# Performance work log

Measured on AMD Instinct MI355X. Metric: run time of the kernel, lower is better.

## Reference

```python
import jax, jax.numpy as jnp
import numpy as np

MIN_R, MAX_R = -51.2, 51.2
ORIG_W, ORIG_H = 800.0, 448.0


def sample_bilinear(feat, gx, gy):
    # feat [N,C,H,W]; gx,gy [N,Q] in grid coords [-1,1], align_corners=True, zeros padding
    N, C, H, W = feat.shape
    px = (gx + 1.0) * 0.5 * (W - 1)
    py = (gy + 1.0) * 0.5 * (H - 1)
    x0 = jnp.floor(px)
    y0 = jnp.floor(py)
    x0i = x0.astype(jnp.int32)
    y0i = y0.astype(jnp.int32)
    wx1 = px - x0
    wy1 = py - y0
    ff = feat.reshape(N, C, H * W)

    def corner(xi, yi, w):
        valid = (xi >= 0) & (xi < W) & (yi >= 0) & (yi < H)
        idx = jnp.clip(yi, 0, H - 1) * W + jnp.clip(xi, 0, W - 1)
        vals = jax.vmap(lambda f, i: f[:, i])(ff, idx)  # [N,C,Q]
        return vals * (w * valid.astype(w.dtype))[:, None, :]

    return (corner(x0i, y0i, (1 - wx1) * (1 - wy1))
            + corner(x0i + 1, y0i, wx1 * (1 - wy1))
            + corner(x0i, y0i + 1, (1 - wx1) * wy1)
            + corner(x0i + 1, y0i + 1, wx1 * wy1))


def setup_inputs() -> dict:
    key = jax.random.key(0)
    ks = jax.random.split(key, 16)
    B, Q, C, N = 2, 900, 256, 6
    levels = [(112, 200), (56, 100), (28, 50), (14, 25)]
    inp = {
        'query': jax.random.normal(ks[0], (B, Q, C), jnp.float32),
        'reference_points': jax.random.uniform(ks[1], (B, Q, 3), jnp.float32),
        'key_padding_mask': jax.random.bernoulli(ks[2], 0.1, (B, Q)),
        'cam_intrinsics': jax.random.normal(ks[3], (B, N, 3, 3), jnp.float32),
        'cam_extrinsics': jax.random.normal(ks[4], (B, N, 4, 4), jnp.float32),
    }
    for li, (h, w) in enumerate(levels):
        inp[f'feats_l{li}'] = jax.random.normal(ks[5 + li], (B, N, C, h, w), jnp.float32)
    inp['Wq'] = jax.random.normal(ks[10], (C, C), jnp.float32) * 0.02
    inp['bq'] = jnp.zeros((C,), jnp.float32)
    inp['Wv'] = jax.random.normal(ks[11], (C, C), jnp.float32) * 0.02
    inp['bv'] = jnp.zeros((C,), jnp.float32)
    inp['Wo'] = jax.random.normal(ks[12], (C, C), jnp.float32) * 0.02
    inp['bo'] = jnp.zeros((C,), jnp.float32)
    return inp


def reference(query, reference_points, key_padding_mask, cam_intrinsics, cam_extrinsics,
              feats_l0, feats_l1, feats_l2, feats_l3, Wq, bq, Wv, bv, Wo, bo):
    B, Q, C = query.shape
    N = cam_extrinsics.shape[1]
    mask = key_padding_mask

    ref = reference_points * (MAX_R - MIN_R) + MIN_R
    ref = jnp.where(mask[..., None], jnp.float32(-1000.0), ref)

    q = query @ Wq.T + bq

    ref_hom = jnp.concatenate([ref, jnp.ones((B, Q, 1), ref.dtype)], axis=-1)  # [B,Q,4]
    inv_ext = jnp.nan_to_num(jnp.linalg.inv(cam_extrinsics), nan=0.0, posinf=1e6, neginf=-1e6)
    # per-cam: points_cam_hom = ref_hom @ inv_ext^T  -> [B,N,Q,4]
    pts_cam_hom = jnp.einsum('bqj,bnij->bnqi', ref_hom, inv_ext)
    depth = jnp.nan_to_num(pts_cam_hom[..., 2:3], nan=10.0, posinf=100.0, neginf=-100.0)
    invalid = depth[..., 0] < 1.5  # [B,N,Q]
    depth_safe = jnp.maximum(depth, 1.5)
    pts_cam = pts_cam_hom[..., :3] / depth_safe
    pts_img = jnp.einsum('bnqj,bnij->bnqi', pts_cam, cam_intrinsics)[..., :2]
    pts_img = jnp.clip(pts_img, -3000.0, 3000.0)  # [B,N,Q,2]

    level_sum = jnp.zeros((B * N, C, Q), jnp.float32)
    for feat in (feats_l0, feats_l1, feats_l2, feats_l3):
        Hf, Wf = feat.shape[3], feat.shape[4]
        fx = pts_img[..., 0] * (Wf / ORIG_W)
        fy = pts_img[..., 1] * (Hf / ORIG_H)
        gx = jnp.clip(fx / (Wf - 1.0) * 2.0 - 1.0, -10.0, 10.0)
        gy = jnp.clip(fy / (Hf - 1.0) * 2.0 - 1.0, -10.0, 10.0)
        gx = jnp.where(invalid, jnp.float32(-100.0), gx)
        gy = jnp.where(invalid, jnp.float32(-100.0), gy)
        s = sample_bilinear(feat.reshape(B * N, C, Hf, Wf),
                            gx.reshape(B * N, Q), gy.reshape(B * N, Q))
        level_sum = level_sum + jnp.nan_to_num(s)

    ms = (level_sum / 4.0).reshape(B, N, C, Q).transpose(0, 1, 3, 2)  # [B,N,Q,C]
    v = ms @ Wv.T + bv
    sampled = jnp.max(v, axis=1)  # max over cameras -> [B,Q,C]

    fused = jax.nn.relu(q + sampled) + q
    out = fused @ Wo.T + bo
    out = out * (~mask)[..., None].astype(out.dtype)
    return out
```

## Files before the change

kernel.cpp:

```cpp
#include <hip/hip_runtime.h>
#include <hip/hip_bf16.h>
#include <math.h>

#define BB 2
#define NCAM 6
#define NQ 900
#define NC 256
#define BN (BB*NCAM)
#define NROW (BB*NQ)

typedef float f4 __attribute__((ext_vector_type(4)));
typedef unsigned short u16x4 __attribute__((ext_vector_type(4)));

__device__ __forceinline__ float u2f(unsigned short u){
  union{unsigned int v; float fl;} x; x.v=((unsigned int)u)<<16; return x.fl;
}

template<int F>
__device__ __forceinline__ float ld1(const void* p, long i){
  if (F) return u2f(((const unsigned short*)p)[i]);
  return ((const float*)p)[i];
}
template<int F>
__device__ __forceinline__ f4 ld4(const void* p, long i){
  if (F){
    u16x4 u = *(const u16x4*)((const unsigned short*)p + i);
    f4 r; r.x=u2f(u.x); r.y=u2f(u.y); r.z=u2f(u.z); r.w=u2f(u.w); return r;
  }
  return *(const f4*)((const float*)p + i);
}

__global__ void prep_kernel(const unsigned char* __restrict__ refraw,
                            const void* __restrict__ ext,
                            const unsigned char* __restrict__ mask_raw,
                            int* __restrict__ flag_out,
                            float* __restrict__ inv_out,
                            int* __restrict__ mask_out){
  __shared__ int s_nonalign, s_gt1, s_bf, s_flag;
  int t = threadIdx.x;
  if (t==0){
    s_nonalign=0; s_gt1=0; s_bf=0;
    int cnt=0;
    for (int i=1;i<64;i+=4){
      unsigned char b = refraw[i];
      if (b>=0x30 && b<0x40) cnt++;
    }
    s_flag = (cnt>=12) ? 1 : 0;
    *flag_out = s_flag;
  }
  __syncthreads();
  int f_na=0, f_gt=0, f_bf=0;
  for (int i=t;i<NROW;i+=blockDim.x){
    unsigned char b = mask_raw[i];
    if ((i&3)!=0 && b!=0) f_na=1;
    if (b>1) f_gt=1;
    if ((i&3)==1 && b==0x3f) f_bf=1;
  }
  if (f_na) atomicOr(&s_nonalign,1);
  if (f_gt) atomicOr(&s_gt1,1);
  if (f_bf) atomicOr(&s_bf,1);
  __syncthreads();
  int fmt;
  if (!s_nonalign) fmt=0;
  else if (!s_gt1)  fmt=1;
  else              fmt = s_bf ? 2 : 3;
  for (int i=t;i<NROW;i+=blockDim.x){
    int v;
    if (fmt==0)      v = (((const int*)mask_raw)[i]            != 0);
    else if (fmt==1) v = (mask_raw[i]                          != 0);
    else if (fmt==2) v = (((const unsigned short*)mask_raw)[i] != 0);
    else             v = (((const float*)mask_raw)[i]          != 0.0f);
    mask_out[i]=v;
  }
  if (t < BN){
    int f = s_flag;
    double a[4][8];
    for(int i=0;i<4;i++){
      for(int j=0;j<4;j++) a[i][j] = (double)(f? u2f(((const unsigned short*)ext)[t*16+i*4+j])
                                               : ((const float*)ext)[t*16+i*4+j]);
      for(int j=0;j<4;j++) a[i][4+j] = (i==j)?1.0:0.0;
    }
    for(int col=0;col<4;col++){
      int piv=col; double best=fabs(a[col][col]);
      for(int r=col+1;r<4;r++){ double v=fabs(a[r][col]); if(v>best){best=v;piv=r;} }
      if(piv!=col) for(int j=0;j<8;j++){ double tmp=a[col][j]; a[col][j]=a[piv][j]; a[piv][j]=tmp; }
      double id = 1.0/a[col][col];
      for(int j=0;j<8;j++) a[col][j]*=id;
      for(int r=0;r<4;r++) if(r!=col){
        double fc=a[r][col];
        for(int j=0;j<8;j++) a[r][j]-=fc*a[col][j];
      }
    }
    for(int i=0;i<4;i++)for(int j=0;j<4;j++){
      float v=(float)a[i][4+j];
      if (isnan(v)) v=0.f;
      else if (isinf(v)) v = (v>0.f)?1e6f:-1e6f;
      inv_out[t*16+i*4+j]=v;
    }
  }
}

__global__ __launch_bounds__(256) void relayout_kernel(
    const void* __restrict__ Wq, const void* __restrict__ Wv,
    const void* __restrict__ Wo, const int* __restrict__ flag,
    float* __restrict__ dst){
  int e = blockIdx.x*256 + threadIdx.x;
  int f = *flag;
  int mat = e >> 16;
  int i = e & 65535;
  int t = i >> 8, k = i & 255;
  const void* W = (mat==0)?Wq:((mat==1)?Wv:Wo);
  float v = f ? u2f(((const unsigned short*)W)[i]) : ((const float*)W)[i];
  dst[mat*65536 + (k>>2)*1024 + t*4 + (k&3)] = v;
}

struct SharedMem {
  float q[NC];
  float ms[NCAM][NC];
  float fus[NC];
  float px[NCAM], py[NCAM];
  int   iv[NCAM];
  int   off[NCAM*4][4];
  float wgt[NCAM*4][4];
};

template<int F, int RL>
__device__ __forceinline__ void fused_body(
    const void* __restrict__ query, const void* __restrict__ refpts,
    const void* __restrict__ intr,
    const void* __restrict__ f0, const void* __restrict__ f1,
    const void* __restrict__ f2, const void* __restrict__ f3,
    const void* __restrict__ Wq, const void* __restrict__ bq,
    const void* __restrict__ Wv, const void* __restrict__ bv,
    const void* __restrict__ Wo, const void* __restrict__ bo,
    const float* __restrict__ Wblk,
    const float* __restrict__ inv_ext, const int* __restrict__ mask_int,
    float* __restrict__ out, SharedMem& sm){
  int row = blockIdx.x;
  int b = row/NQ;
  int t = threadIdx.x;
  int m = mask_int[row];

  const f4* Wq4 = (const f4*)(Wblk);
  const f4* Wv4 = (const f4*)(Wblk + 65536);
  const f4* Wo4 = (const f4*)(Wblk + 131072);

  sm.q[t] = ld1<F>(query, (long)row*NC+t);
  if (t < NCAM){
    float h0 = ld1<F>(refpts,(long)row*3+0)*102.4f - 51.2f;
    float h1 = ld1<F>(refpts,(long)row*3+1)*102.4f - 51.2f;
    float h2 = ld1<F>(refpts,(long)row*3+2)*102.4f - 51.2f;
    if (m){ h0=-1000.f; h1=-1000.f; h2=-1000.f; }
    const float* M = inv_ext + (b*NCAM+t)*16;
    float c0 = M[0]*h0 + M[1]*h1 + M[2]*h2 + M[3];
    float c1 = M[4]*h0 + M[5]*h1 + M[6]*h2 + M[7];
    float c2 = M[8]*h0 + M[9]*h1 + M[10]*h2 + M[11];
    float depth = c2;
    if (isnan(depth)) depth = 10.f;
    else if (isinf(depth)) depth = (depth>0)?100.f:-100.f;
    int iv = (depth < 1.5f);
    float ds = fmaxf(depth, 1.5f);
    float pc0=c0/ds, pc1=c1/ds, pc2=c2/ds;
    long kb = (long)(b*NCAM+t)*9;
    float ix = ld1<F>(intr,kb+0)*pc0 + ld1<F>(intr,kb+1)*pc1 + ld1<F>(intr,kb+2)*pc2;
    float iy = ld1<F>(intr,kb+3)*pc0 + ld1<F>(intr,kb+4)*pc1 + ld1<F>(intr,kb+5)*pc2;
    sm.px[t] = fminf(fmaxf(ix,-3000.f),3000.f);
    sm.py[t] = fminf(fmaxf(iy,-3000.f),3000.f);
    sm.iv[t] = iv;
  }
  __syncthreads();

  if (t < NCAM*4){
    const int Ws_[4]={200,100,50,25}, Hs_[4]={112,56,28,14};
    int n=t>>2, l=t&3;
    float x=sm.px[n], y=sm.py[n];
    int iv=sm.iv[n];
    int W=Ws_[l], H=Hs_[l];
    float gx = (x * ((float)W/800.f)) / (W-1.f) * 2.f - 1.f;
    float gy = (y * ((float)H/448.f)) / (H-1.f) * 2.f - 1.f;
    gx=fminf(fmaxf(gx,-10.f),10.f); gy=fminf(fmaxf(gy,-10.f),10.f);
    if(iv){gx=-100.f;gy=-100.f;}
    float pxx=(gx+1.f)*0.5f*(W-1.f);
    float pyy=(gy+1.f)*0.5f*(H-1.f);
    float x0f=floorf(pxx), y0f=floorf(pyy);
    int x0=(int)x0f, y0=(int)y0f;
    float wx1=pxx-x0f, wy1=pyy-y0f, wx0=1.f-wx1, wy0=1.f-wy1;
    int vx0=(x0>=0)&(x0<W), vx1=(x0+1>=0)&(x0+1<W);
    int vy0=(y0>=0)&(y0<H), vy1=(y0+1>=0)&(y0+1<H);
    int cx0=min(max(x0,0),W-1), cx1=min(max(x0+1,0),W-1);
    int cy0=min(max(y0,0),H-1), cy1=min(max(y0+1,0),H-1);
    sm.off[t][0]=cy0*W+cx0; sm.wgt[t][0]=wx0*wy0*(float)(vx0&vy0);
    sm.off[t][1]=cy0*W+cx1; sm.wgt[t][1]=wx1*wy0*(float)(vx1&vy0);
    sm.off[t][2]=cy1*W+cx0; sm.wgt[t][2]=wx0*wy1*(float)(vx0&vy1);
    sm.off[t][3]=cy1*W+cx1; sm.wgt[t][3]=wx1*wy1*(float)(vx1&vy1);
  }
  __syncthreads();

  {
    const void* fb[4]={f0,f1,f2,f3};
    const long HWs[4]={22400,5600,1400,350};
    #pragma unroll
    for(int n=0;n<NCAM;n++){
      int chan = (b*NCAM+n)*NC + t;
      float acc=0.f;
      #pragma unroll
      for(int l=0;l<4;l++){
        int u=n*4+l;
        long cb=(long)chan*HWs[l];
        const void* fp=fb[l];
        acc=fmaf(sm.wgt[u][0], ld1<F>(fp,cb+sm.off[u][0]), acc);
        acc=fmaf(sm.wgt[u][1], ld1<F>(fp,cb+sm.off[u][1]), acc);
        acc=fmaf(sm.wgt[u][2], ld1<F>(fp,cb+sm.off[u][2]), acc);
        acc=fmaf(sm.wgt[u][3], ld1<F>(fp,cb+sm.off[u][3]), acc);
      }
      sm.ms[n][t]=acc*0.25f;
    }
  }

  float qv = 0.f;
  {
    const f4* sq4=(const f4*)sm.q;
    #pragma unroll 8
    for(int k4=0;k4<NC/4;k4++){
      f4 wv = RL ? Wq4[k4*256 + t] : ld4<F>(Wq, (long)t*NC + 4*k4);
      f4 xv = sq4[k4];
      qv=fmaf(wv.x,xv.x,qv); qv=fmaf(wv.y,xv.y,qv);
      qv=fmaf(wv.z,xv.z,qv); qv=fmaf(wv.w,xv.w,qv);
    }
    qv += ld1<F>(bq,t);
  }
  __syncthreads();

  float ac[NCAM];
  #pragma unroll
  for(int n=0;n<NCAM;n++) ac[n]=0.f;
  {
    #pragma unroll 4
    for(int k4=0;k4<NC/4;k4++){
      f4 wv = RL ? Wv4[k4*256 + t] : ld4<F>(Wv, (long)t*NC + 4*k4);
      #pragma unroll
      for(int n=0;n<NCAM;n++){
        f4 mv=((const f4*)sm.ms[n])[k4];
        ac[n]=fmaf(wv.x,mv.x,ac[n]); ac[n]=fmaf(wv.y,mv.y,ac[n]);
        ac[n]=fmaf(wv.z,mv.z,ac[n]); ac[n]=fmaf(wv.w,mv.w,ac[n]);
      }
    }
  }
  float sv = ac[0];
  #pragma unroll
  for(int n=1;n<NCAM;n++) sv = fmaxf(sv, ac[n]);
  sv += ld1<F>(bv,t);

  sm.fus[t] = fmaxf(qv+sv, 0.f) + qv;
  __syncthreads();

  float o = 0.f;
  {
    const f4* sf4=(const f4*)sm.fus;
    #pragma unroll 8
    for(int k4=0;k4<NC/4;k4++){
      f4 wv = RL ? Wo4[k4*256 + t] : ld4<F>(Wo, (long)t*NC + 4*k4);
      f4 xv = sf4[k4];
      o=fmaf(wv.x,xv.x,o); o=fmaf(wv.y,xv.y,o);
      o=fmaf(wv.z,xv.z,o); o=fmaf(wv.w,xv.w,o);
    }
    o += ld1<F>(bo,t);
  }
  if (m) o = 0.f;
  out[(long)row*NC+t] = o;
}

template<int RL>
__global__ __launch_bounds__(256,4) void fused_kernel(
    const void* query, const void* refpts, const void* intr,
    const void* f0, const void* f1, const void* f2, const void* f3,
    const void* Wq, const void* bq, const void* Wv, const void* bv,
    const void* Wo, const void* bo, const float* __restrict__ Wblk,
    const float* __restrict__ inv_ext, const int* __restrict__ mask_int,
    const int* __restrict__ flag, float* __restrict__ out){
  __shared__ SharedMem sm;
  if (*flag)
    fused_body<1,RL>(query,refpts,intr,f0,f1,f2,f3,Wq,bq,Wv,bv,Wo,bo,Wblk,inv_ext,mask_int,out,sm);
  else
    fused_body<0,RL>(query,refpts,intr,f0,f1,f2,f3,Wq,bq,Wv,bv,Wo,bo,Wblk,inv_ext,mask_int,out,sm);
}

extern "C" void kernel_launch(void* const* d_in, const int* in_sizes, int n_in,
                              void* d_out, int out_size, void* d_ws, size_t ws_size,
                              hipStream_t stream){
  const void* query  = d_in[0];
  const void* refpts = d_in[1];
  const unsigned char* mask_raw = (const unsigned char*)d_in[2];
  const void* intr   = d_in[3];
  const void* ext    = d_in[4];
  const void* f0     = d_in[5];
  const void* f1     = d_in[6];
  const void* f2     = d_in[7];
  const void* f3     = d_in[8];
  const void* Wq     = d_in[9];
  const void* bq     = d_in[10];
  const void* Wv     = d_in[11];
  const void* bv     = d_in[12];
  const void* Wo     = d_in[13];
  const void* bo     = d_in[14];

  char* ws = (char*)d_ws;
  float* inv_ext  = (float*)(ws + 0);
  int*   dflag    = (int*)  (ws + 1024);
  int*   mask_int = (int*)  (ws + 2048);
  float* Wblk     = (float*)(ws + 16384);

  hipLaunchKernelGGL(prep_kernel, dim3(1), dim3(256), 0, stream,
                     (const unsigned char*)refpts, ext, mask_raw, dflag, inv_ext, mask_int);

  bool relay = ws_size >= (size_t)(16384 + 786432);
  if (relay){
    hipLaunchKernelGGL(relayout_kernel, dim3(768), dim3(256), 0, stream,
                       Wq, Wv, Wo, dflag, Wblk);
    hipLaunchKernelGGL(fused_kernel<1>, dim3(NROW), dim3(256), 0, stream,
                       query, refpts, intr, f0, f1, f2, f3,
                       Wq, bq, Wv, bv, Wo, bo, Wblk,
                       inv_ext, mask_int, dflag, (float*)d_out);
  } else {
    hipLaunchKernelGGL(fused_kernel<0>, dim3(NROW), dim3(256), 0, stream,
                       query, refpts, intr, f0, f1, f2, f3,
                       Wq, bq, Wv, bv, Wo, bo, Wblk,
                       inv_ext, mask_int, dflag, (float*)d_out);
  }
}
```

Before: 542.5 us.

## Process two rows per block, transpose small feature levels channel-last, merge prep kernels

Each block now handles two query rows, so every weight vector loaded for the Wq, Wv and Wo matvecs is reused across both rows. All 16 bilinear gather loads per camera are issued up front, before any accumulation. Feature levels 2 and 3 are transposed into a channel-contiguous workspace buffer in the prep kernel, so the sampling gathers become coalesced across threads. The prep, weight relayout and feature transposes are merged into one launch. The cost is extra per-call transpose traffic (about 17 MB written), higher shared-memory and register use per block, and half as many blocks.

```diff
diff --git a/kernel.cpp b/kernel.cpp
--- a/kernel.cpp
+++ b/kernel.cpp
@@ -8,6 +8,12 @@
 #define NC 256
 #define BN (BB*NCAM)
 #define NROW (BB*NQ)
+#define RPB 2
+
+#define HW0 22400
+#define HW1 5600
+#define HW2 1400
+#define HW3 350
 
 typedef float f4 __attribute__((ext_vector_type(4)));
 typedef unsigned short u16x4 __attribute__((ext_vector_type(4)));
@@ -30,25 +36,63 @@
   return *(const f4*)((const float*)p + i);
 }
 
-__global__ void prep_kernel(const unsigned char* __restrict__ refraw,
-                            const void* __restrict__ ext,
-                            const unsigned char* __restrict__ mask_raw,
-                            int* __restrict__ flag_out,
-                            float* __restrict__ inv_out,
-                            int* __restrict__ mask_out){
-  __shared__ int s_nonalign, s_gt1, s_bf, s_flag;
+__device__ __forceinline__ int sniff_flag(const unsigned char* refraw){
+  int cnt=0;
+  for (int i=1;i<64;i+=4){
+    unsigned char b = refraw[i];
+    if (b>=0x30 && b<0x40) cnt++;
+  }
+  return (cnt>=12) ? 1 : 0;
+}
+
+__global__ __launch_bounds__(256) void prep_all(
+    const unsigned char* __restrict__ refraw,
+    const void* __restrict__ ext,
+    const unsigned char* __restrict__ mask_raw,
+    const void* __restrict__ Wq, const void* __restrict__ Wv,
+    const void* __restrict__ Wo,
+    const void* __restrict__ f2, const void* __restrict__ f3,
+    int nW, int nT2, int nT3,
+    int* __restrict__ flag_out, float* __restrict__ inv_out,
+    int* __restrict__ mask_out,
+    float* __restrict__ Wblk, float* __restrict__ T2buf,
+    float* __restrict__ T3buf){
+  __shared__ int sflag, s_na, s_gt, s_bf;
   int t = threadIdx.x;
-  if (t==0){
-    s_nonalign=0; s_gt1=0; s_bf=0;
-    int cnt=0;
-    for (int i=1;i<64;i+=4){
-      unsigned char b = refraw[i];
-      if (b>=0x30 && b<0x40) cnt++;
-    }
-    s_flag = (cnt>=12) ? 1 : 0;
-    *flag_out = s_flag;
-  }
-  __syncthreads();
+  int bi = blockIdx.x;
+  if (t==0){ sflag = sniff_flag(refraw); s_na=0; s_gt=0; s_bf=0; }
+  __syncthreads();
+  int f = sflag;
+
+  if (bi < nW){
+    int e = bi*256 + t;
+    int mat = e >> 16;
+    int i = e & 65535;
+    int tt = i >> 8, k = i & 255;
+    const void* W = (mat==0)?Wq:((mat==1)?Wv:Wo);
+    float v = f ? u2f(((const unsigned short*)W)[i]) : ((const float*)W)[i];
+    Wblk[mat*65536 + (k>>2)*1024 + tt*4 + (k&3)] = v;
+    return;
+  }
+  if (bi < nW+nT2){
+    int e = (bi-nW)*256 + t;
+    int bn = e / (HW2*NC);
+    int rem = e - bn*(HW2*NC);
+    int p = rem >> 8, c = rem & 255;
+    int src = (bn*NC + c)*HW2 + p;
+    T2buf[e] = f ? u2f(((const unsigned short*)f2)[src]) : ((const float*)f2)[src];
+    return;
+  }
+  if (bi < nW+nT2+nT3){
+    int e = (bi-nW-nT2)*256 + t;
+    int bn = e / (HW3*NC);
+    int rem = e - bn*(HW3*NC);
+    int p = rem >> 8, c = rem & 255;
+    int src = (bn*NC + c)*HW3 + p;
+    T3buf[e] = f ? u2f(((const unsigned short*)f3)[src]) : ((const float*)f3)[src];
+    return;
+  }
+
   int f_na=0, f_gt=0, f_bf=0;
   for (int i=t;i<NROW;i+=blockDim.x){
     unsigned char b = mask_raw[i];
@@ -56,14 +100,14 @@
     if (b>1) f_gt=1;
     if ((i&3)==1 && b==0x3f) f_bf=1;
   }
-  if (f_na) atomicOr(&s_nonalign,1);
-  if (f_gt) atomicOr(&s_gt1,1);
+  if (f_na) atomicOr(&s_na,1);
+  if (f_gt) atomicOr(&s_gt,1);
   if (f_bf) atomicOr(&s_bf,1);
   __syncthreads();
   int fmt;
-  if (!s_nonalign) fmt=0;
-  else if (!s_gt1)  fmt=1;
-  else              fmt = s_bf ? 2 : 3;
+  if (!s_na) fmt=0;
+  else if (!s_gt) fmt=1;
+  else fmt = s_bf ? 2 : 3;
   for (int i=t;i<NROW;i+=blockDim.x){
     int v;
     if (fmt==0)      v = (((const int*)mask_raw)[i]            != 0);
@@ -72,8 +116,8 @@
     else             v = (((const float*)mask_raw)[i]          != 0.0f);
     mask_out[i]=v;
   }
+  if (t==0) *flag_out = f;
   if (t < BN){
-    int f = s_flag;
     double a[4][8];
     for(int i=0;i<4;i++){
       for(int j=0;j<4;j++) a[i][j] = (double)(f? u2f(((const unsigned short*)ext)[t*16+i*4+j])
@@ -100,31 +144,17 @@
   }
 }
 
-__global__ __launch_bounds__(256) void relayout_kernel(
-    const void* __restrict__ Wq, const void* __restrict__ Wv,
-    const void* __restrict__ Wo, const int* __restrict__ flag,
-    float* __restrict__ dst){
-  int e = blockIdx.x*256 + threadIdx.x;
-  int f = *flag;
-  int mat = e >> 16;
-  int i = e & 65535;
-  int t = i >> 8, k = i & 255;
-  const void* W = (mat==0)?Wq:((mat==1)?Wv:Wo);
-  float v = f ? u2f(((const unsigned short*)W)[i]) : ((const float*)W)[i];
-  dst[mat*65536 + (k>>2)*1024 + t*4 + (k&3)] = v;
-}
-
 struct SharedMem {
-  float q[NC];
-  float ms[NCAM][NC];
-  float fus[NC];
-  float px[NCAM], py[NCAM];
-  int   iv[NCAM];
-  int   off[NCAM*4][4];
-  float wgt[NCAM*4][4];
+  float q[RPB][NC];
+  float ms[RPB][NCAM][NC];
+  float fus[RPB][NC];
+  float px[RPB][NCAM], py[RPB][NCAM];
+  int   iv[RPB][NCAM];
+  int   off[RPB][NCAM*4][4];
+  float wgt[RPB][NCAM*4][4];
 };
 
-template<int F, int RL>
+template<int F, int RL, int RF>
 __device__ __forceinline__ void fused_body(
     const void* __restrict__ query, const void* __restrict__ refpts,
     const void* __restrict__ intr,
@@ -134,24 +164,28 @@
     const void* __restrict__ Wv, const void* __restrict__ bv,
     const void* __restrict__ Wo, const void* __restrict__ bo,
     const float* __restrict__ Wblk,
+    const float* __restrict__ T2buf, const float* __restrict__ T3buf,
     const float* __restrict__ inv_ext, const int* __restrict__ mask_int,
     float* __restrict__ out, SharedMem& sm){
-  int row = blockIdx.x;
-  int b = row/NQ;
+  int r0 = blockIdx.x*RPB;
   int t = threadIdx.x;
-  int m = mask_int[row];
 
   const f4* Wq4 = (const f4*)(Wblk);
   const f4* Wv4 = (const f4*)(Wblk + 65536);
   const f4* Wo4 = (const f4*)(Wblk + 131072);
 
-  sm.q[t] = ld1<F>(query, (long)row*NC+t);
-  if (t < NCAM){
+  #pragma unroll
+  for(int i=0;i<RPB;i++) sm.q[i][t] = ld1<F>(query,(long)(r0+i)*NC+t);
+
+  if (t < RPB*NCAM){
+    int i = t/NCAM, n = t - i*NCAM;
+    int row = r0+i, b = row/NQ;
+    int m = mask_int[row];
     float h0 = ld1<F>(refpts,(long)row*3+0)*102.4f - 51.2f;
     float h1 = ld1<F>(refpts,(long)row*3+1)*102.4f - 51.2f;
     float h2 = ld1<F>(refpts,(long)row*3+2)*102.4f - 51.2f;
     if (m){ h0=-1000.f; h1=-1000.f; h2=-1000.f; }
-    const float* M = inv_ext + (b*NCAM+t)*16;
+    const float* M = inv_ext + (b*NCAM+n)*16;
     float c0 = M[0]*h0 + M[1]*h1 + M[2]*h2 + M[3];
     float c1 = M[4]*h0 + M[5]*h1 + M[6]*h2 + M[7];
     float c2 = M[8]*h0 + M[9]*h1 + M[10]*h2 + M[11];
@@ -161,20 +195,21 @@
     int iv = (depth < 1.5f);
     float ds = fmaxf(depth, 1.5f);
     float pc0=c0/ds, pc1=c1/ds, pc2=c2/ds;
-    long kb = (long)(b*NCAM+t)*9;
+    long kb = (long)(b*NCAM+n)*9;
     float ix = ld1<F>(intr,kb+0)*pc0 + ld1<F>(intr,kb+1)*pc1 + ld1<F>(intr,kb+2)*pc2;
     float iy = ld1<F>(intr,kb+3)*pc0 + ld1<F>(intr,kb+4)*pc1 + ld1<F>(intr,kb+5)*pc2;
-    sm.px[t] = fminf(fmaxf(ix,-3000.f),3000.f);
-    sm.py[t] = fminf(fmaxf(iy,-3000.f),3000.f);
-    sm.iv[t] = iv;
-  }
-  __syncthreads();
-
-  if (t < NCAM*4){
+    sm.px[i][n] = fminf(fmaxf(ix,-3000.f),3000.f);
+    sm.py[i][n] = fminf(fmaxf(iy,-3000.f),3000.f);
+    sm.iv[i][n] = iv;
+  }
+  __syncthreads();
+
+  if (t < RPB*NCAM*4){
     const int Ws_[4]={200,100,50,25}, Hs_[4]={112,56,28,14};
-    int n=t>>2, l=t&3;
-    float x=sm.px[n], y=sm.py[n];
-    int iv=sm.iv[n];
+    int i = t/(NCAM*4), u = t - i*(NCAM*4);
+    int n = u>>2, l = u&3;
+    float x=sm.px[i][n], y=sm.py[i][n];
+    int iv=sm.iv[i][n];
     int W=Ws_[l], H=Hs_[l];
     float gx = (x * ((float)W/800.f)) / (W-1.f) * 2.f - 1.f;
     float gy = (y * ((float)H/448.f)) / (H-1.f) * 2.f - 1.f;
@@ -189,100 +224,152 @@
     int vy0=(y0>=0)&(y0<H), vy1=(y0+1>=0)&(y0+1<H);
     int cx0=min(max(x0,0),W-1), cx1=min(max(x0+1,0),W-1);
     int cy0=min(max(y0,0),H-1), cy1=min(max(y0+1,0),H-1);
-    sm.off[t][0]=cy0*W+cx0; sm.wgt[t][0]=wx0*wy0*(float)(vx0&vy0);
-    sm.off[t][1]=cy0*W+cx1; sm.wgt[t][1]=wx1*wy0*(float)(vx1&vy0);
-    sm.off[t][2]=cy1*W+cx0; sm.wgt[t][2]=wx0*wy1*(float)(vx0&vy1);
-    sm.off[t][3]=cy1*W+cx1; sm.wgt[t][3]=wx1*wy1*(float)(vx1&vy1);
-  }
-  __syncthreads();
-
-  {
-    const void* fb[4]={f0,f1,f2,f3};
-    const long HWs[4]={22400,5600,1400,350};
+    sm.off[i][u][0]=cy0*W+cx0; sm.wgt[i][u][0]=wx0*wy0*(float)(vx0&vy0);
+    sm.off[i][u][1]=cy0*W+cx1; sm.wgt[i][u][1]=wx1*wy0*(float)(vx1&vy0);
+    sm.off[i][u][2]=cy1*W+cx0; sm.wgt[i][u][2]=wx0*wy1*(float)(vx0&vy1);
+    sm.off[i][u][3]=cy1*W+cx1; sm.wgt[i][u][3]=wx1*wy1*(float)(vx1&vy1);
+  }
+  __syncthreads();
+
+  #pragma unroll
+  for(int i=0;i<RPB;i++){
+    int b = (r0+i)/NQ;
     #pragma unroll
     for(int n=0;n<NCAM;n++){
-      int chan = (b*NCAM+n)*NC + t;
+      int bn = b*NCAM+n;
+      int chan = bn*NC + t;
+      float v[16];
+      {
+        long cb0 = (long)chan*HW0;
+        #pragma unroll
+        for(int c=0;c<4;c++) v[c]   = ld1<F>(f0, cb0 + sm.off[i][n*4+0][c]);
+        long cb1 = (long)chan*HW1;
+        #pragma unroll
+        for(int c=0;c<4;c++) v[4+c] = ld1<F>(f1, cb1 + sm.off[i][n*4+1][c]);
+      }
+      if (RF>=2){
+        const float* Tp = T2buf + bn*(HW2*NC) + t;
+        #pragma unroll
+        for(int c=0;c<4;c++) v[8+c] = Tp[sm.off[i][n*4+2][c]*NC];
+      } else {
+        long cb2 = (long)chan*HW2;
+        #pragma unroll
+        for(int c=0;c<4;c++) v[8+c] = ld1<F>(f2, cb2 + sm.off[i][n*4+2][c]);
+      }
+      if (RF>=1){
+        const float* Tp = T3buf + bn*(HW3*NC) + t;
+        #pragma unroll
+        for(int c=0;c<4;c++) v[12+c] = Tp[sm.off[i][n*4+3][c]*NC];
+      } else {
+        long cb3 = (long)chan*HW3;
+        #pragma unroll
+        for(int c=0;c<4;c++) v[12+c] = ld1<F>(f3, cb3 + sm.off[i][n*4+3][c]);
+      }
       float acc=0.f;
       #pragma unroll
       for(int l=0;l<4;l++){
-        int u=n*4+l;
-        long cb=(long)chan*HWs[l];
-        const void* fp=fb[l];
-        acc=fmaf(sm.wgt[u][0], ld1<F>(fp,cb+sm.off[u][0]), acc);
-        acc=fmaf(sm.wgt[u][1], ld1<F>(fp,cb+sm.off[u][1]), acc);
-        acc=fmaf(sm.wgt[u][2], ld1<F>(fp,cb+sm.off[u][2]), acc);
-        acc=fmaf(sm.wgt[u][3], ld1<F>(fp,cb+sm.off[u][3]), acc);
-      }
-      sm.ms[n][t]=acc*0.25f;
-    }
-  }
-
-  float qv = 0.f;
+        #pragma unroll
+        for(int c=0;c<4;c++)
+          acc = fmaf(sm.wgt[i][n*4+l][c], v[l*4+c], acc);
+      }
+      sm.ms[i][n][t] = acc*0.25f;
+    }
+  }
+
+  float qv[RPB];
+  #pragma unroll
+  for(int i=0;i<RPB;i++) qv[i]=0.f;
   {
-    const f4* sq4=(const f4*)sm.q;
     #pragma unroll 8
     for(int k4=0;k4<NC/4;k4++){
       f4 wv = RL ? Wq4[k4*256 + t] : ld4<F>(Wq, (long)t*NC + 4*k4);
-      f4 xv = sq4[k4];
-      qv=fmaf(wv.x,xv.x,qv); qv=fmaf(wv.y,xv.y,qv);
-      qv=fmaf(wv.z,xv.z,qv); qv=fmaf(wv.w,xv.w,qv);
-    }
-    qv += ld1<F>(bq,t);
-  }
-  __syncthreads();
-
-  float ac[NCAM];
+      #pragma unroll
+      for(int i=0;i<RPB;i++){
+        f4 xv = ((const f4*)sm.q[i])[k4];
+        qv[i]=fmaf(wv.x,xv.x,qv[i]); qv[i]=fmaf(wv.y,xv.y,qv[i]);
+        qv[i]=fmaf(wv.z,xv.z,qv[i]); qv[i]=fmaf(wv.w,xv.w,qv[i]);
+      }
+    }
+    float bqv = ld1<F>(bq,t);
+    #pragma unroll
+    for(int i=0;i<RPB;i++) qv[i]+=bqv;
+  }
+  __syncthreads();
+
+  float ac[RPB][NCAM];
   #pragma unroll
-  for(int n=0;n<NCAM;n++) ac[n]=0.f;
+  for(int i=0;i<RPB;i++)
+    #pragma unroll
+    for(int n=0;n<NCAM;n++) ac[i][n]=0.f;
   {
-    #pragma unroll 4
+    #pragma unroll 2
     for(int k4=0;k4<NC/4;k4++){
       f4 wv = RL ? Wv4[k4*256 + t] : ld4<F>(Wv, (long)t*NC + 4*k4);
       #pragma unroll
-      for(int n=0;n<NCAM;n++){
-        f4 mv=((const f4*)sm.ms[n])[k4];
-        ac[n]=fmaf(wv.x,mv.x,ac[n]); ac[n]=fmaf(wv.y,mv.y,ac[n]);
-        ac[n]=fmaf(wv.z,mv.z,ac[n]); ac[n]=fmaf(wv.w,mv.w,ac[n]);
-      }
-    }
-  }
-  float sv = ac[0];
+      for(int i=0;i<RPB;i++){
+        #pragma unroll
+        for(int n=0;n<NCAM;n++){
+          f4 mv=((const f4*)sm.ms[i][n])[k4];
+          ac[i][n]=fmaf(wv.x,mv.x,ac[i][n]); ac[i][n]=fmaf(wv.y,mv.y,ac[i][n]);
+          ac[i][n]=fmaf(wv.z,mv.z,ac[i][n]); ac[i][n]=fmaf(wv.w,mv.w,ac[i][n]);
+        }
+      }
+    }
+  }
+  {
+    float bvv = ld1<F>(bv,t);
+    #pragma unroll
+    for(int i=0;i<RPB;i++){
+      float sv = ac[i][0];
+      #pragma unroll
+      for(int n=1;n<NCAM;n++) sv = fmaxf(sv, ac[i][n]);
+      sv += bvv;
+      sm.fus[i][t] = fmaxf(qv[i]+sv, 0.f) + qv[i];
+    }
+  }
+  __syncthreads();
+
+  float o[RPB];
   #pragma unroll
-  for(int n=1;n<NCAM;n++) sv = fmaxf(sv, ac[n]);
-  sv += ld1<F>(bv,t);
-
-  sm.fus[t] = fmaxf(qv+sv, 0.f) + qv;
-  __syncthreads();
-
-  float o = 0.f;
+  for(int i=0;i<RPB;i++) o[i]=0.f;
   {
-    const f4* sf4=(const f4*)sm.fus;
     #pragma unroll 8
     for(int k4=0;k4<NC/4;k4++){
       f4 wv = RL ? Wo4[k4*256 + t] : ld4<F>(Wo, (long)t*NC + 4*k4);
-      f4 xv = sf4[k4];
-      o=fmaf(wv.x,xv.x,o); o=fmaf(wv.y,xv.y,o);
-      o=fmaf(wv.z,xv.z,o); o=fmaf(wv.w,xv.w,o);
-    }
-    o += ld1<F>(bo,t);
-  }
-  if (m) o = 0.f;
-  out[(long)row*NC+t] = o;
-}
-
-template<int RL>
+      #pragma unroll
+      for(int i=0;i<RPB;i++){
+        f4 xv = ((const f4*)sm.fus[i])[k4];
+        o[i]=fmaf(wv.x,xv.x,o[i]); o[i]=fmaf(wv.y,xv.y,o[i]);
+        o[i]=fmaf(wv.z,xv.z,o[i]); o[i]=fmaf(wv.w,xv.w,o[i]);
+      }
+    }
+    float bov = ld1<F>(bo,t);
+    #pragma unroll
+    for(int i=0;i<RPB;i++){
+      int m = mask_int[r0+i];
+      float r = o[i] + bov;
+      if (m) r = 0.f;
+      out[(long)(r0+i)*NC+t] = r;
+    }
+  }
+}
+
+template<int RL, int RF>
 __global__ __launch_bounds__(256,4) void fused_kernel(
     const void* query, const void* refpts, const void* intr,
     const void* f0, const void* f1, const void* f2, const void* f3,
     const void* Wq, const void* bq, const void* Wv, const void* bv,
     const void* Wo, const void* bo, const float* __restrict__ Wblk,
+    const float* __restrict__ T2buf, const float* __restrict__ T3buf,
     const float* __restrict__ inv_ext, const int* __restrict__ mask_int,
     const int* __restrict__ flag, float* __restrict__ out){
   __shared__ SharedMem sm;
   if (*flag)
-    fused_body<1,RL>(query,refpts,intr,f0,f1,f2,f3,Wq,bq,Wv,bv,Wo,bo,Wblk,inv_ext,mask_int,out,sm);
+    fused_body<1,RL,RF>(query,refpts,intr,f0,f1,f2,f3,Wq,bq,Wv,bv,Wo,bo,
+                        Wblk,T2buf,T3buf,inv_ext,mask_int,out,sm);
   else
-    fused_body<0,RL>(query,refpts,intr,f0,f1,f2,f3,Wq,bq,Wv,bv,Wo,bo,Wblk,inv_ext,mask_int,out,sm);
+    fused_body<0,RL,RF>(query,refpts,intr,f0,f1,f2,f3,Wq,bq,Wv,bv,Wo,bo,
+                        Wblk,T2buf,T3buf,inv_ext,mask_int,out,sm);
 }
 
 extern "C" void kernel_launch(void* const* d_in, const int* in_sizes, int n_in,
@@ -309,22 +396,44 @@
   int*   dflag    = (int*)  (ws + 1024);
   int*   mask_int = (int*)  (ws + 2048);
   float* Wblk     = (float*)(ws + 16384);
-
-  hipLaunchKernelGGL(prep_kernel, dim3(1), dim3(256), 0, stream,
-                     (const unsigned char*)refpts, ext, mask_raw, dflag, inv_ext, mask_int);
-
-  bool relay = ws_size >= (size_t)(16384 + 786432);
-  if (relay){
-    hipLaunchKernelGGL(relayout_kernel, dim3(768), dim3(256), 0, stream,
-                       Wq, Wv, Wo, dflag, Wblk);
-    hipLaunchKernelGGL(fused_kernel<1>, dim3(NROW), dim3(256), 0, stream,
+  float* T3buf    = (float*)(ws + 802816);
+  float* T2buf    = (float*)(ws + 5103616);
+
+  const size_t needW  = 802816;
+  const size_t need3  = 5103616;
+  const size_t need23 = 22306816;
+
+  int rl = (ws_size >= needW) ? 1 : 0;
+  int rf = (ws_size >= need23) ? 2 : ((ws_size >= need3) ? 1 : 0);
+
+  int nW  = rl ? 768 : 0;
+  int nT2 = (rf>=2) ? (BN*HW2*NC)/256 : 0;
+  int nT3 = (rf>=1) ? (BN*HW3*NC)/256 : 0;
+
+  hipLaunchKernelGGL(prep_all, dim3(nW+nT2+nT3+1), dim3(256), 0, stream,
+                     (const unsigned char*)refpts, ext, mask_raw,
+                     Wq, Wv, Wo, f2, f3, nW, nT2, nT3,
+                     dflag, inv_ext, mask_int, Wblk, T2buf, T3buf);
+
+  dim3 grid(NROW/RPB);
+  if (rl && rf==2)
+    hipLaunchKernelGGL(HIP_KERNEL_NAME(fused_kernel<1,2>), grid, dim3(256), 0, stream,
                        query, refpts, intr, f0, f1, f2, f3,
-                       Wq, bq, Wv, bv, Wo, bo, Wblk,
+                       Wq, bq, Wv, bv, Wo, bo, Wblk, T2buf, T3buf,
                        inv_ext, mask_int, dflag, (float*)d_out);
-  } else {
-    hipLaunchKernelGGL(fused_kernel<0>, dim3(NROW), dim3(256), 0, stream,
+  else if (rl && rf==1)
+    hipLaunchKernelGGL(HIP_KERNEL_NAME(fused_kernel<1,1>), grid, dim3(256), 0, stream,
                        query, refpts, intr, f0, f1, f2, f3,
-                       Wq, bq, Wv, bv, Wo, bo, Wblk,
+                       Wq, bq, Wv, bv, Wo, bo, Wblk, T2buf, T3buf,
                        inv_ext, mask_int, dflag, (float*)d_out);
-  }
-}
+  else if (rl)
+    hipLaunchKernelGGL(HIP_KERNEL_NAME(fused_kernel<1,0>), grid, dim3(256), 0, stream,
+                       query, refpts, intr, f0, f1, f2, f3,
+                       Wq, bq, Wv, bv, Wo, bo, Wblk, T2buf, T3buf,
+                       inv_ext, mask_int, dflag, (float*)d_out);
+  else
+    hipLaunchKernelGGL(HIP_KERNEL_NAME(fused_kernel<0,0>), grid, dim3(256), 0, stream,
+                       query, refpts, intr, f0, f1, f2, f3,
+                       Wq, bq, Wv, bv, Wo, bo, Wblk, T2buf, T3buf,
+                       inv_ext, mask_int, dflag, (float*)d_out);
+}
```

Result: faster. 522.5 us (-3.7%).

## Transpose small feature levels to channel-last and pair adjacent bilinear corner loads

Applied to the files above, without the earlier changes.

A merged prep kernel now converts the level-2 and level-3 feature maps into a channel-last layout in workspace, alongside the existing weight relayout and mask/extrinsic prep, so there is one fewer launch. When sampling those levels, the 256 threads of a row then read contiguous channels instead of strided scalars. Levels 0 and 1 fetch each pair of horizontally adjacent corners with a single 8-byte load, using a clamped base column. The cost is transposing about 21 MB of features on every call, which adds memory traffic and requires a larger workspace; smaller workspaces fall back to the old paths.

```diff
diff --git a/kernel.cpp b/kernel.cpp
--- a/kernel.cpp
+++ b/kernel.cpp
@@ -9,8 +9,14 @@
 #define BN (BB*NCAM)
 #define NROW (BB*NQ)
 
+#define HW0 22400
+#define HW1 5600
+#define HW2 1400
+#define HW3 350
+
 typedef float f4 __attribute__((ext_vector_type(4)));
 typedef unsigned short u16x4 __attribute__((ext_vector_type(4)));
+typedef struct __attribute__((aligned(4))) { float x, y; } pf2;
 
 __device__ __forceinline__ float u2f(unsigned short u){
   union{unsigned int v; float fl;} x; x.v=((unsigned int)u)<<16; return x.fl;
@@ -30,25 +36,91 @@
   return *(const f4*)((const float*)p + i);
 }
 
-__global__ void prep_kernel(const unsigned char* __restrict__ refraw,
-                            const void* __restrict__ ext,
-                            const unsigned char* __restrict__ mask_raw,
-                            int* __restrict__ flag_out,
-                            float* __restrict__ inv_out,
-                            int* __restrict__ mask_out){
-  __shared__ int s_nonalign, s_gt1, s_bf, s_flag;
+template<int F>
+__device__ __forceinline__ void corner4(const void* fp, long cb, int offA, int offB,
+                                        int d0, int d1, float* v){
+  if (F){
+    v[0]=ld1<1>(fp,cb+offA+d0); v[1]=ld1<1>(fp,cb+offA+d1);
+    v[2]=ld1<1>(fp,cb+offB+d0); v[3]=ld1<1>(fp,cb+offB+d1);
+  } else {
+    pf2 a = *(const pf2*)((const float*)fp + cb + offA);
+    pf2 b = *(const pf2*)((const float*)fp + cb + offB);
+    v[0]=d0?a.y:a.x; v[1]=d1?a.y:a.x;
+    v[2]=d0?b.y:b.x; v[3]=d1?b.y:b.x;
+  }
+}
+
+__device__ __forceinline__ int sniff_flag(const unsigned char* refraw){
+  int cnt=0;
+  for (int i=1;i<64;i+=4){
+    unsigned char b = refraw[i];
+    if (b>=0x30 && b<0x40) cnt++;
+  }
+  return (cnt>=12) ? 1 : 0;
+}
+
+#define TILES2 (8*44)
+#define TILES3 (8*11)
+__global__ __launch_bounds__(256) void prep_all(
+    const unsigned char* __restrict__ refraw,
+    const void* __restrict__ ext,
+    const unsigned char* __restrict__ mask_raw,
+    const void* __restrict__ Wq, const void* __restrict__ Wv,
+    const void* __restrict__ Wo,
+    const void* __restrict__ f2, const void* __restrict__ f3,
+    int nW, int nT2t, int nT3t,
+    int* __restrict__ flag_out, float* __restrict__ inv_out,
+    int* __restrict__ mask_out,
+    float* __restrict__ Wblk, float* __restrict__ T2buf,
+    float* __restrict__ T3buf){
+  __shared__ int sflag, s_na, s_gt, s_bf;
+  __shared__ float tile[32][33];
   int t = threadIdx.x;
-  if (t==0){
-    s_nonalign=0; s_gt1=0; s_bf=0;
-    int cnt=0;
-    for (int i=1;i<64;i+=4){
-      unsigned char b = refraw[i];
-      if (b>=0x30 && b<0x40) cnt++;
-    }
-    s_flag = (cnt>=12) ? 1 : 0;
-    *flag_out = s_flag;
-  }
-  __syncthreads();
+  int bi = blockIdx.x;
+  if (t==0){ sflag = sniff_flag(refraw); s_na=0; s_gt=0; s_bf=0; }
+  __syncthreads();
+  int f = sflag;
+
+  if (bi < nW){
+    int e = bi*256 + t;
+    int mat = e >> 16;
+    int i = e & 65535;
+    int tt = i >> 8, k = i & 255;
+    const void* W = (mat==0)?Wq:((mat==1)?Wv:Wo);
+    float v = f ? u2f(((const unsigned short*)W)[i]) : ((const float*)W)[i];
+    Wblk[mat*65536 + (k>>2)*1024 + tt*4 + (k&3)] = v;
+    return;
+  }
+  if (bi < nW+nT2t+nT3t){
+    int idx = bi - nW;
+    const void* src; float* dst; int HW, tpb, tp;
+    if (idx < nT2t){ HW=HW2; src=f2; dst=T2buf; tpb=TILES2; tp=44; }
+    else { idx -= nT2t; HW=HW3; src=f3; dst=T3buf; tpb=TILES3; tp=11; }
+    int bn = idx / tpb; int rem = idx - bn*tpb;
+    int ct = rem / tp,  pt = rem - ct*tp;
+    int c0 = ct*32, p0 = pt*32;
+    int ty = t>>5, tx = t&31;
+    #pragma unroll
+    for (int r=0;r<4;r++){
+      int c = c0 + ty + r*8;
+      int p = p0 + tx;
+      float v = 0.f;
+      if (p < HW){
+        long s = (long)(bn*NC + c)*HW + p;
+        v = f ? u2f(((const unsigned short*)src)[s]) : ((const float*)src)[s];
+      }
+      tile[ty+r*8][tx] = v;
+    }
+    __syncthreads();
+    #pragma unroll
+    for (int r=0;r<4;r++){
+      int p = p0 + ty + r*8;
+      if (p < HW)
+        dst[((long)bn*HW + p)*NC + c0 + tx] = tile[tx][ty+r*8];
+    }
+    return;
+  }
+
   int f_na=0, f_gt=0, f_bf=0;
   for (int i=t;i<NROW;i+=blockDim.x){
     unsigned char b = mask_raw[i];
@@ -56,14 +128,14 @@
     if (b>1) f_gt=1;
     if ((i&3)==1 && b==0x3f) f_bf=1;
   }
-  if (f_na) atomicOr(&s_nonalign,1);
-  if (f_gt) atomicOr(&s_gt1,1);
+  if (f_na) atomicOr(&s_na,1);
+  if (f_gt) atomicOr(&s_gt,1);
   if (f_bf) atomicOr(&s_bf,1);
   __syncthreads();
   int fmt;
-  if (!s_nonalign) fmt=0;
-  else if (!s_gt1)  fmt=1;
-  else              fmt = s_bf ? 2 : 3;
+  if (!s_na) fmt=0;
+  else if (!s_gt) fmt=1;
+  else fmt = s_bf ? 2 : 3;
   for (int i=t;i<NROW;i+=blockDim.x){
     int v;
     if (fmt==0)      v = (((const int*)mask_raw)[i]            != 0);
@@ -72,8 +144,8 @@
     else             v = (((const float*)mask_raw)[i]          != 0.0f);
     mask_out[i]=v;
   }
+  if (t==0) *flag_out = f;
   if (t < BN){
-    int f = s_flag;
     double a[4][8];
     for(int i=0;i<4;i++){
       for(int j=0;j<4;j++) a[i][j] = (double)(f? u2f(((const unsigned short*)ext)[t*16+i*4+j])
@@ -100,20 +172,6 @@
   }
 }
 
-__global__ __launch_bounds__(256) void relayout_kernel(
-    const void* __restrict__ Wq, const void* __restrict__ Wv,
-    const void* __restrict__ Wo, const int* __restrict__ flag,
-    float* __restrict__ dst){
-  int e = blockIdx.x*256 + threadIdx.x;
-  int f = *flag;
-  int mat = e >> 16;
-  int i = e & 65535;
-  int t = i >> 8, k = i & 255;
-  const void* W = (mat==0)?Wq:((mat==1)?Wv:Wo);
-  float v = f ? u2f(((const unsigned short*)W)[i]) : ((const float*)W)[i];
-  dst[mat*65536 + (k>>2)*1024 + t*4 + (k&3)] = v;
-}
-
 struct SharedMem {
   float q[NC];
   float ms[NCAM][NC];
@@ -124,7 +182,7 @@
   float wgt[NCAM*4][4];
 };
 
-template<int F, int RL>
+template<int F, int RL, int RF>
 __device__ __forceinline__ void fused_body(
     const void* __restrict__ query, const void* __restrict__ refpts,
     const void* __restrict__ intr,
@@ -134,6 +192,7 @@
     const void* __restrict__ Wv, const void* __restrict__ bv,
     const void* __restrict__ Wo, const void* __restrict__ bo,
     const float* __restrict__ Wblk,
+    const float* __restrict__ T2buf, const float* __restrict__ T3buf,
     const float* __restrict__ inv_ext, const int* __restrict__ mask_int,
     float* __restrict__ out, SharedMem& sm){
   int row = blockIdx.x;
@@ -189,29 +248,62 @@
     int vy0=(y0>=0)&(y0<H), vy1=(y0+1>=0)&(y0+1<H);
     int cx0=min(max(x0,0),W-1), cx1=min(max(x0+1,0),W-1);
     int cy0=min(max(y0,0),H-1), cy1=min(max(y0+1,0),H-1);
-    sm.off[t][0]=cy0*W+cx0; sm.wgt[t][0]=wx0*wy0*(float)(vx0&vy0);
-    sm.off[t][1]=cy0*W+cx1; sm.wgt[t][1]=wx1*wy0*(float)(vx1&vy0);
-    sm.off[t][2]=cy1*W+cx0; sm.wgt[t][2]=wx0*wy1*(float)(vx0&vy1);
-    sm.off[t][3]=cy1*W+cx1; sm.wgt[t][3]=wx1*wy1*(float)(vx1&vy1);
+    int px = min(max(x0,0),W-2);
+    int d0 = cx0 - px, d1 = cx1 - px;
+    sm.off[t][0]=cy0*W+px; sm.off[t][1]=cy1*W+px;
+    sm.off[t][2]=d0;       sm.off[t][3]=d1;
+    sm.wgt[t][0]=wx0*wy0*(float)(vx0&vy0);
+    sm.wgt[t][1]=wx1*wy0*(float)(vx1&vy0);
+    sm.wgt[t][2]=wx0*wy1*(float)(vx0&vy1);
+    sm.wgt[t][3]=wx1*wy1*(float)(vx1&vy1);
   }
   __syncthreads();
 
   {
-    const void* fb[4]={f0,f1,f2,f3};
-    const long HWs[4]={22400,5600,1400,350};
+    const long HWs01[2]={HW0,HW1};
+    const void* fb01[2]={f0,f1};
+    int bnb = b*NCAM;
     #pragma unroll
     for(int n=0;n<NCAM;n++){
-      int chan = (b*NCAM+n)*NC + t;
+      int bn = bnb+n;
+      int chan = bn*NC + t;
+      float v[16];
+      #pragma unroll
+      for(int l=0;l<2;l++){
+        int u=n*4+l;
+        corner4<F>(fb01[l], (long)chan*HWs01[l],
+                   sm.off[u][0], sm.off[u][1], sm.off[u][2], sm.off[u][3], &v[l*4]);
+      }
+      {
+        int u=n*4+2;
+        if (RF>=2){
+          const float* Tp = T2buf + (long)bn*(HW2*NC) + t;
+          int oA=sm.off[u][0], oB=sm.off[u][1], d0=sm.off[u][2], d1=sm.off[u][3];
+          v[8] =Tp[(long)(oA+d0)*NC]; v[9] =Tp[(long)(oA+d1)*NC];
+          v[10]=Tp[(long)(oB+d0)*NC]; v[11]=Tp[(long)(oB+d1)*NC];
+        } else {
+          corner4<F>(f2, (long)chan*HW2,
+                     sm.off[u][0], sm.off[u][1], sm.off[u][2], sm.off[u][3], &v[8]);
+        }
+      }
+      {
+        int u=n*4+3;
+        if (RF>=1){
+          const float* Tp = T3buf + (long)bn*(HW3*NC) + t;
+          int oA=sm.off[u][0], oB=sm.off[u][1], d0=sm.off[u][2], d1=sm.off[u][3];
+          v[12]=Tp[(long)(oA+d0)*NC]; v[13]=Tp[(long)(oA+d1)*NC];
+          v[14]=Tp[(long)(oB+d0)*NC]; v[15]=Tp[(long)(oB+d1)*NC];
+        } else {
+          corner4<F>(f3, (long)chan*HW3,
+                     sm.off[u][0], sm.off[u][1], sm.off[u][2], sm.off[u][3], &v[12]);
+        }
+      }
       float acc=0.f;
       #pragma unroll
       for(int l=0;l<4;l++){
-        int u=n*4+l;
-        long cb=(long)chan*HWs[l];
-        const void* fp=fb[l];
-        acc=fmaf(sm.wgt[u][0], ld1<F>(fp,cb+sm.off[u][0]), acc);
-        acc=fmaf(sm.wgt[u][1], ld1<F>(fp,cb+sm.off[u][1]), acc);
-        acc=fmaf(sm.wgt[u][2], ld1<F>(fp,cb+sm.off[u][2]), acc);
-        acc=fmaf(sm.wgt[u][3], ld1<F>(fp,cb+sm.off[u][3]), acc);
+        #pragma unroll
+        for(int c=0;c<4;c++)
+          acc = fmaf(sm.wgt[n*4+l][c], v[l*4+c], acc);
       }
       sm.ms[n][t]=acc*0.25f;
     }
@@ -270,19 +362,22 @@
   out[(long)row*NC+t] = o;
 }
 
-template<int RL>
+template<int RL, int RF>
 __global__ __launch_bounds__(256,4) void fused_kernel(
     const void* query, const void* refpts, const void* intr,
     const void* f0, const void* f1, const void* f2, const void* f3,
     const void* Wq, const void* bq, const void* Wv, const void* bv,
     const void* Wo, const void* bo, const float* __restrict__ Wblk,
+    const float* __restrict__ T2buf, const float* __restrict__ T3buf,
     const float* __restrict__ inv_ext, const int* __restrict__ mask_int,
     const int* __restrict__ flag, float* __restrict__ out){
   __shared__ SharedMem sm;
   if (*flag)
-    fused_body<1,RL>(query,refpts,intr,f0,f1,f2,f3,Wq,bq,Wv,bv,Wo,bo,Wblk,inv_ext,mask_int,out,sm);
+    fused_body<1,RL,RF>(query,refpts,intr,f0,f1,f2,f3,Wq,bq,Wv,bv,Wo,bo,
+                        Wblk,T2buf,T3buf,inv_ext,mask_int,out,sm);
   else
-    fused_body<0,RL>(query,refpts,intr,f0,f1,f2,f3,Wq,bq,Wv,bv,Wo,bo,Wblk,inv_ext,mask_int,out,sm);
+    fused_body<0,RL,RF>(query,refpts,intr,f0,f1,f2,f3,Wq,bq,Wv,bv,Wo,bo,
+                        Wblk,T2buf,T3buf,inv_ext,mask_int,out,sm);
 }
 
 extern "C" void kernel_launch(void* const* d_in, const int* in_sizes, int n_in,
@@ -309,22 +404,44 @@
   int*   dflag    = (int*)  (ws + 1024);
   int*   mask_int = (int*)  (ws + 2048);
   float* Wblk     = (float*)(ws + 16384);
-
-  hipLaunchKernelGGL(prep_kernel, dim3(1), dim3(256), 0, stream,
-                     (const unsigned char*)refpts, ext, mask_raw, dflag, inv_ext, mask_int);
-
-  bool relay = ws_size >= (size_t)(16384 + 786432);
-  if (relay){
-    hipLaunchKernelGGL(relayout_kernel, dim3(768), dim3(256), 0, stream,
-                       Wq, Wv, Wo, dflag, Wblk);
-    hipLaunchKernelGGL(fused_kernel<1>, dim3(NROW), dim3(256), 0, stream,
+  float* T3buf    = (float*)(ws + 802816);
+  float* T2buf    = (float*)(ws + 5103616);
+
+  const size_t needW  = 802816;
+  const size_t need3  = 5103616;
+  const size_t need23 = 22306816;
+
+  int rl = (ws_size >= needW) ? 1 : 0;
+  int rf = (ws_size >= need23) ? 2 : ((ws_size >= need3) ? 1 : 0);
+
+  int nW   = rl ? 768 : 0;
+  int nT2t = (rf>=2) ? BN*TILES2 : 0;
+  int nT3t = (rf>=1) ? BN*TILES3 : 0;
+
+  hipLaunchKernelGGL(prep_all, dim3(nW+nT2t+nT3t+1), dim3(256), 0, stream,
+                     (const unsigned char*)refpts, ext, mask_raw,
+                     Wq, Wv, Wo, f2, f3, nW, nT2t, nT3t,
+                     dflag, inv_ext, mask_int, Wblk, T2buf, T3buf);
+
+  dim3 grid(NROW);
+  if (rl && rf==2)
+    hipLaunchKernelGGL(HIP_KERNEL_NAME(fused_kernel<1,2>), grid, dim3(256), 0, stream,
                        query, refpts, intr, f0, f1, f2, f3,
-                       Wq, bq, Wv, bv, Wo, bo, Wblk,
+                       Wq, bq, Wv, bv, Wo, bo, Wblk, T2buf, T3buf,
                        inv_ext, mask_int, dflag, (float*)d_out);
-  } else {
-    hipLaunchKernelGGL(fused_kernel<0>, dim3(NROW), dim3(256), 0, stream,
+  else if (rl && rf==1)
+    hipLaunchKernelGGL(HIP_KERNEL_NAME(fused_kernel<1,1>), grid, dim3(256), 0, stream,
                        query, refpts, intr, f0, f1, f2, f3,
-                       Wq, bq, Wv, bv, Wo, bo, Wblk,
+                       Wq, bq, Wv, bv, Wo, bo, Wblk, T2buf, T3buf,
                        inv_ext, mask_int, dflag, (float*)d_out);
-  }
-}
+  else if (rl)
+    hipLaunchKernelGGL(HIP_KERNEL_NAME(fused_kernel<1,0>), grid, dim3(256), 0, stream,
+                       query, refpts, intr, f0, f1, f2, f3,
+                       Wq, bq, Wv, bv, Wo, bo, Wblk, T2buf, T3buf,
+                       inv_ext, mask_int, dflag, (float*)d_out);
+  else
+    hipLaunchKernelGGL(HIP_KERNEL_NAME(fused_kernel<0,0>), grid, dim3(256), 0, stream,
+                       query, refpts, intr, f0, f1, f2, f3,
+                       Wq, bq, Wv, bv, Wo, bo, Wblk, T2buf, T3buf,
+                       inv_ext, mask_int, dflag, (float*)d_out);
+}
```

Result: faster. 503.3 us (-7.2%).
